# Kernel tuning notes

Measured on AMD Instinct MI355X. Metric: run time of the kernel, lower is better.

Reference implementation:

```python
import jax, jax.numpy as jnp
import numpy as np

# Dims: batch=2, seqlen=L=384, d_inner=d=384, d_state=s=384, dt_rank=r=384, d_conv=4.
# NOTE: the original torch module only runs when L == d_inner == d_state == dt_rank
# (see its broadcasting in SelectiveScan and the Linear layer plumbing); we reproduce
# that exact (quirky) broadcast faithfully.
B_, L_, D_, S_, R_, K_ = 2, 384, 384, 384, 384, 4


def setup_inputs() -> dict:
    key = jax.random.key(0)
    ks = jax.random.split(key, 9)
    f32 = jnp.float32
    return {
        "x": jax.random.normal(ks[0], (B_, L_, D_), f32),
        "A_log": jax.random.normal(ks[1], (D_, S_), f32) * 0.02,
        "D": jax.random.normal(ks[2], (D_,), f32) * 0.02,
        "dt_w": jax.random.normal(ks[3], (D_, R_), f32) * 0.02,
        "dt_b": jax.random.normal(ks[4], (D_,), f32) * 0.02,
        "B_w": jax.random.normal(ks[5], (S_, D_), f32) * (1.0 / np.sqrt(D_)),
        "C_w": jax.random.normal(ks[6], (S_, D_), f32) * (1.0 / np.sqrt(D_)),
        "conv_w": jax.random.normal(ks[7], (D_, 1, K_), f32) * (1.0 / np.sqrt(K_)),
        "conv_b": jnp.zeros((D_,), f32),
    }


def _forward(x, A_log, D, dt_w, dt_b, B_w, C_w, conv_w, conv_b):
    b, L, d = x.shape
    A = -jnp.exp(A_log)                       # (d, s)
    dt = jax.nn.softplus(x @ dt_w.T + dt_b)   # (b, L, d)
    x_dbl = x @ B_w.T                         # (b, L, s)
    Bm = x_dbl @ B_w.T                        # (b, L, s)  (module applies B_proj twice)
    Cm = x_dbl @ C_w.T                        # (b, L, s)
    # causal depthwise conv1d: pad (k-1) on the left == torch pad k-1 then [:, :, :L]
    xc = jax.lax.conv_general_dilated(
        x.transpose(0, 2, 1), conv_w, (1,), [(conv_w.shape[-1] - 1, 0)],
        feature_group_count=d, dimension_numbers=("NCH", "OIH", "NCH"))
    xc = xc + conv_b[None, :, None]
    u = jax.nn.silu(xc.transpose(0, 2, 1))    # (b, L, d)
    # selective scan (faithful to the torch SelectiveScan broadcasting)
    deltaA = jnp.exp(dt[..., None] * A[None, None])          # (b, L, d, s)
    deltaB_u = dt[..., None] * Bm[:, None, :, :] * u[..., None]  # (b, L, d, s), needs L==d

    def step(h, inp):
        dA_i, dBu_i, C_i, u_i = inp
        h = dA_i * h + dBu_i                  # (b, d, s)
        y = jnp.sum(h * C_i[:, None, :], -1) + u_i * D  # (b, d)
        return h, y

    h0 = jnp.zeros((b, d, deltaA.shape[-1]), x.dtype)
    xs = (deltaA.transpose(1, 0, 2, 3), deltaB_u.transpose(1, 0, 2, 3),
          Cm.transpose(1, 0, 2), u.transpose(1, 0, 2))
    _, ys = jax.lax.scan(step, h0, xs)        # ys: (L, b, d)
    return ys.transpose(1, 0, 2)


def reference(x, A_log, D, dt_w, dt_b, B_w, C_w, conv_w, conv_b):
    return _forward(x, A_log, D, dt_w, dt_b, B_w, C_w, conv_w, conv_b)
```

## Files before the change

kernel.cpp:

```cpp
#include <hip/hip_runtime.h>
#include <math.h>

#define B_SZ 2
#define L_SZ 384
#define D_SZ 384
#define S_SZ 384
#define BLK_ELEMS (L_SZ * D_SZ)
#define TOT_ELEMS (B_SZ * L_SZ * D_SZ)
#define LOG2E 1.4426950408889634f

typedef __attribute__((ext_vector_type(8))) short bf16x8;
typedef __attribute__((ext_vector_type(4))) float f32x4;
typedef __attribute__((ext_vector_type(2))) unsigned int u32x2;

__device__ __forceinline__ float fexp2(float x) {
  return __builtin_amdgcn_exp2f(x);
}
__device__ __forceinline__ float softplus_f(float z) {
  return (z > 20.f) ? z : log1pf(__expf(z));
}
__device__ __forceinline__ unsigned short f2bf(float f) {
  unsigned int u = __float_as_uint(f);
  return (unsigned short)((u + 0x7FFFu + ((u >> 16) & 1u)) >> 16);
}
#define PIPELINE_FENCE() asm volatile("" ::: "memory")

__device__ __forceinline__ bf16x8 cvt8(const float* p) {
  const f32x4 v0 = *(const f32x4*)p;
  const f32x4 v1 = *(const f32x4*)(p + 4);
  union { unsigned int u[4]; bf16x8 v; } r;
  asm("v_cvt_pk_bf16_f32 %0, %1, %2" : "=v"(r.u[0]) : "v"(v0[0]), "v"(v0[1]));
  asm("v_cvt_pk_bf16_f32 %0, %1, %2" : "=v"(r.u[1]) : "v"(v0[2]), "v"(v0[3]));
  asm("v_cvt_pk_bf16_f32 %0, %1, %2" : "=v"(r.u[2]) : "v"(v1[0]), "v"(v1[1]));
  asm("v_cvt_pk_bf16_f32 %0, %1, %2" : "=v"(r.u[3]) : "v"(v1[2]), "v"(v1[3]));
  return r.v;
}

template <int CTRL>
__device__ __forceinline__ float dpp_mov(float v) {
  return __int_as_float(
      __builtin_amdgcn_update_dpp(0, __float_as_int(v), CTRL, 0xF, 0xF, true));
}

__device__ __forceinline__ float fold_xor16(float r) {
#if __has_builtin(__builtin_amdgcn_permlane16_swap)
  const unsigned ru = __float_as_uint(r);
  u32x2 p = __builtin_amdgcn_permlane16_swap(ru, ru, false, false);
  return __uint_as_float(p[0]) + __uint_as_float(p[1]);
#else
  return r + __shfl_xor(r, 16, 64);
#endif
}
__device__ __forceinline__ float fold_xor32(float r) {
#if __has_builtin(__builtin_amdgcn_permlane32_swap)
  const unsigned ru = __float_as_uint(r);
  u32x2 p = __builtin_amdgcn_permlane32_swap(ru, ru, false, false);
  return __uint_as_float(p[0]) + __uint_as_float(p[1]);
#else
  return r + __shfl_xor(r, 32, 64);
#endif
}

template <int MODE>
__global__ __launch_bounds__(128, 2) void mfma_dual_gemm(
    const void* __restrict__ Av, const float* __restrict__ W1,
    const float* __restrict__ W2, const float* __restrict__ bias,
    float* __restrict__ O1, unsigned short* __restrict__ O2) {
  __shared__ unsigned short sA[32 * 392];
  __shared__ unsigned short sW1[16 * 392];
  __shared__ unsigned short sW2[16 * 392];

  const int t = threadIdx.x;
  const int wv = t >> 6;
  const int lane = t & 63;
  const int nt = blockIdx.x;
  const int mrow = blockIdx.y;

  const float* W1b = W1 + nt * 16 * 384;
  const float* W2b = W2 + nt * 16 * 384;

  if constexpr (MODE == 1) {
    const float* Ab = (const float*)Av + mrow * 32 * 384;
#pragma unroll
    for (int it = 0; it < 12; ++it) {
      const int id = t + it * 128;
      const int row = id / 48, col = id - row * 48;
      *(bf16x8*)&sA[row * 392 + col * 8] = cvt8(Ab + id * 8);
    }
  } else {
    const unsigned short* Ab = (const unsigned short*)Av + mrow * 32 * 384;
#pragma unroll
    for (int it = 0; it < 12; ++it) {
      const int id = t + it * 128;
      const int row = id / 48, col = id - row * 48;
      *(bf16x8*)&sA[row * 392 + col * 8] = *(const bf16x8*)(Ab + id * 8);
    }
  }
#pragma unroll
  for (int it = 0; it < 6; ++it) {
    const int id = t + it * 128;
    const int row = id / 48, col = id - row * 48;
    *(bf16x8*)&sW1[row * 392 + col * 8] = cvt8(W1b + id * 8);
    *(bf16x8*)&sW2[row * 392 + col * 8] = cvt8(W2b + id * 8);
  }
  __syncthreads();

  const int rc = lane & 15;
  const int quad = lane >> 4;
  bf16x8 af[12], w1f[12], w2f[12];
#pragma unroll
  for (int kt = 0; kt < 12; ++kt) {
    af[kt] = *(const bf16x8*)&sA[(wv * 16 + rc) * 392 + quad * 8 + kt * 32];
    w1f[kt] = *(const bf16x8*)&sW1[rc * 392 + quad * 8 + kt * 32];
    w2f[kt] = *(const bf16x8*)&sW2[rc * 392 + quad * 8 + kt * 32];
  }
  PIPELINE_FENCE();
  f32x4 acc1 = {0.f, 0.f, 0.f, 0.f};
  f32x4 acc2 = {0.f, 0.f, 0.f, 0.f};
#pragma unroll
  for (int kt = 0; kt < 12; ++kt) {
    acc1 = __builtin_amdgcn_mfma_f32_16x16x32_bf16(af[kt], w1f[kt], acc1, 0, 0, 0);
    acc2 = __builtin_amdgcn_mfma_f32_16x16x32_bf16(af[kt], w2f[kt], acc2, 0, 0, 0);
  }
  const int col = nt * 16 + rc;
  const int row0 = mrow * 32 + wv * 16 + quad * 4;
  if constexpr (MODE == 1) {
    const float bb = bias[col];
#pragma unroll
    for (int r = 0; r < 4; ++r) {
      O1[(row0 + r) * 384 + col] = softplus_f(acc1[r] + bb);
      O2[(row0 + r) * 384 + col] = f2bf(acc2[r]);
    }
  } else {
#pragma unroll
    for (int r = 0; r < 4; ++r) {
      O1[(row0 + r) * 384 + col] = acc1[r];
      O2[(row0 + r) * 384 + col] = f2bf(acc2[r]);
    }
  }
}

__global__ __launch_bounds__(256) void conv_tr_kernel(
    const float* __restrict__ x, const float* __restrict__ cw,
    const float* __restrict__ cb, const float* __restrict__ dt,
    float* __restrict__ u, float* __restrict__ dt_t,
    float* __restrict__ dtu_t) {
  __shared__ float Tdt[32][33];
  __shared__ float Tdu[32][33];
  const int tx = threadIdx.x;
  const int ty = threadIdx.y;
  const int b = blockIdx.z;
  const int i0 = blockIdx.y * 32;
  const int l0 = blockIdx.x * 32;
  const int gi = i0 + tx;
  const float cbv = cb[gi];
  const float cw0 = cw[gi * 4 + 0], cw1 = cw[gi * 4 + 1];
  const float cw2 = cw[gi * 4 + 2], cw3 = cw[gi * 4 + 3];
#pragma unroll
  for (int r = 0; r < 4; ++r) {
    const int l = l0 + ty + 8 * r;
    float acc = cbv;
    const float x3 = x[(b * L_SZ + l) * D_SZ + gi];
    const float x2 = (l >= 1) ? x[(b * L_SZ + l - 1) * D_SZ + gi] : 0.f;
    const float x1 = (l >= 2) ? x[(b * L_SZ + l - 2) * D_SZ + gi] : 0.f;
    const float x0 = (l >= 3) ? x[(b * L_SZ + l - 3) * D_SZ + gi] : 0.f;
    acc = fmaf(x0, cw0, acc);
    acc = fmaf(x1, cw1, acc);
    acc = fmaf(x2, cw2, acc);
    acc = fmaf(x3, cw3, acc);
    const float uv = acc / (1.f + __expf(-acc));
    const int off = (b * L_SZ + l) * D_SZ + gi;
    u[off] = uv;
    const float dtv = dt[off];
    Tdt[ty + 8 * r][tx] = dtv;
    Tdu[ty + 8 * r][tx] = dtv * uv;
  }
  __syncthreads();
#pragma unroll
  for (int r = 0; r < 4; ++r) {
    const int il = ty + 8 * r;
    const int off = (b * D_SZ + i0 + il) * L_SZ + l0 + tx;
    dt_t[off] = Tdt[tx][il];
    dtu_t[off] = Tdu[tx][il];
  }
}

struct CChunk {
  unsigned int c[8];
};
struct SChunk {
  f32x4 d0, d1, u0, u1;
};

#define LOAD_CHUNK(K, B0, B1, B2)                                              \
  {                                                                            \
    asm volatile("global_load_ushort %0, %1, off" : "=v"(K.c[0]) : "v"(B0));   \
    asm volatile("global_load_ushort %0, %1, off offset:768"                   \
                 : "=v"(K.c[1]) : "v"(B0));                                    \
    asm volatile("global_load_ushort %0, %1, off offset:1536"                  \
                 : "=v"(K.c[2]) : "v"(B0));                                    \
    asm volatile("global_load_ushort %0, %1, off" : "=v"(K.c[3]) : "v"(B1));   \
    asm volatile("global_load_ushort %0, %1, off offset:768"                   \
                 : "=v"(K.c[4]) : "v"(B1));                                    \
    asm volatile("global_load_ushort %0, %1, off offset:1536"                  \
                 : "=v"(K.c[5]) : "v"(B1));                                    \
    asm volatile("global_load_ushort %0, %1, off" : "=v"(K.c[6]) : "v"(B2));   \
    asm volatile("global_load_ushort %0, %1, off offset:768"                   \
                 : "=v"(K.c[7]) : "v"(B2));                                    \
  }

#define WAIT_CHUNK(K)                                                          \
  asm volatile("s_waitcnt vmcnt(16)"                                           \
               : "+v"(K.c[0]), "+v"(K.c[1]), "+v"(K.c[2]), "+v"(K.c[3]),       \
                 "+v"(K.c[4]), "+v"(K.c[5]), "+v"(K.c[6]), "+v"(K.c[7]))

#define SLOAD_CHUNK(S, SDT, SDU)                                               \
  asm volatile("s_load_dwordx4 %0, %4, 0x0\n\t"                                \
               "s_load_dwordx4 %1, %4, 0x10\n\t"                               \
               "s_load_dwordx4 %2, %5, 0x0\n\t"                                \
               "s_load_dwordx4 %3, %5, 0x10"                                   \
               : "=&s"(S.d0), "=&s"(S.d1), "=&s"(S.u0), "=&s"(S.u1)            \
               : "s"(SDT), "s"(SDU));

#define SWAIT(S)                                                               \
  asm volatile("s_waitcnt lgkmcnt(0)"                                          \
               : "+s"(S.d0), "+s"(S.d1), "+s"(S.u0), "+s"(S.u1))

#define ADV_BASES()                                                            \
  { cb0 += 3072; cb1 += 3072; cb2 += 3072; }
#define SADV()                                                                 \
  { sdt += 8; sdu += 8; }

__global__ __launch_bounds__(64, 4) void scan_kernel(
    const float* __restrict__ A_log, const float* __restrict__ dt_t,
    const float* __restrict__ dtu_t, const float* __restrict__ Bm,
    const unsigned short* __restrict__ Cmbf, float* __restrict__ part) {
  const int bid = blockIdx.x;
  const int xcd = bid & 7;
  const int slot = bid >> 3;
  const int sid = xcd * 96 + slot / 6;
  const int w = slot % 6;
  const int lane = threadIdx.x;
  const int b = sid / D_SZ;
  const int i = sid % D_SZ;
  const int j = w * 64 + lane;

  const float a2 = -__expf(A_log[i * S_SZ + j]) * LOG2E;
  const float bw = Bm[(b * D_SZ + i) * S_SZ + j];
  float h = 0.f;

  const float* sdt = dt_t + (b * D_SZ + i) * L_SZ;
  const float* sdu = dtu_t + (b * D_SZ + i) * L_SZ;
  const unsigned short* cmrow = Cmbf + b * BLK_ELEMS + j;
  const unsigned short* cb0 = cmrow;
  const unsigned short* cb1 = cmrow + 3 * S_SZ;
  const unsigned short* cb2 = cmrow + 6 * S_SZ;

  const int sq = (((lane >> 3) & 1) << 2) | (((lane >> 2) & 1) << 1) | (lane & 1);
  const bool storer = (lane & 0x32) == 0;
  float* pstore = part + ((w * B_SZ + b) * D_SZ + i) * L_SZ + sq;

  asm volatile("" :: "v"(a2), "v"(bw));
  asm volatile("s_waitcnt vmcnt(0)");

  auto compute_chunk = [&](CChunk& K, SChunk& S) {
    float acc[8];
    const float dts[8] = {S.d0[0], S.d0[1], S.d0[2], S.d0[3],
                          S.d1[0], S.d1[1], S.d1[2], S.d1[3]};
    const float dus[8] = {S.u0[0], S.u0[1], S.u0[2], S.u0[3],
                          S.u1[0], S.u1[1], S.u1[2], S.u1[3]};
#pragma unroll
    for (int s = 0; s < 8; ++s) {
      const float e = fexp2(dts[s] * a2);
      h = fmaf(e, h, bw * dus[s]);
      acc[s] = h * __uint_as_float(K.c[s] << 16);
    }
    {
      const bool hi = (lane & 8) != 0;
#pragma unroll
      for (int q = 0; q < 4; ++q) {
        const float keep = hi ? acc[q + 4] : acc[q];
        const float send = hi ? acc[q] : acc[q + 4];
        acc[q] = keep + dpp_mov<0x140>(send);
      }
    }
    {
      const bool hi = (lane & 4) != 0;
#pragma unroll
      for (int q = 0; q < 2; ++q) {
        const float keep = hi ? acc[q + 2] : acc[q];
        const float send = hi ? acc[q] : acc[q + 2];
        acc[q] = keep + dpp_mov<0x141>(send);
      }
    }
    {
      const bool hi = (lane & 1) != 0;
      const float keep = hi ? acc[1] : acc[0];
      const float send = hi ? acc[0] : acc[1];
      acc[0] = keep + dpp_mov<0xB1>(send);
    }
    float r = acc[0];
    r += dpp_mov<0x4E>(r);
    r = fold_xor16(r);
    r = fold_xor32(r);
    if (storer) *pstore = r;
    pstore += 8;
  };

  CChunk K0, K1, K2;
  SChunk S0, S1;
  LOAD_CHUNK(K0, cb0, cb1, cb2);
  ADV_BASES();
  LOAD_CHUNK(K1, cb0, cb1, cb2);
  ADV_BASES();
  SLOAD_CHUNK(S0, sdt, sdu);
  SADV();

#define STEP(KC, SC, SN)                                                       \
  LOAD_CHUNK(KC, cb0, cb1, cb2);                                               \
  ADV_BASES();                                                                 \
  WAIT_CHUNK(KC##_wait);                                                       \
  SWAIT(SC);                                                                   \
  SLOAD_CHUNK(SN, sdt, sdu);                                                   \
  SADV();                                                                      \
  compute_chunk(KC##_wait, SC);

#pragma unroll 1
  for (int it = 0; it < 8; ++it) {
    { CChunk& K2_wait = K0; STEP(K2, S0, S1); }
    { CChunk& K0_wait = K1; STEP(K0, S1, S0); }
    { CChunk& K1_wait = K2; STEP(K1, S0, S1); }
    { CChunk& K2_wait = K0; STEP(K2, S1, S0); }
    { CChunk& K0_wait = K1; STEP(K0, S0, S1); }
    { CChunk& K1_wait = K2; STEP(K1, S1, S0); }
  }
#undef STEP
}

__global__ __launch_bounds__(256) void combine_kernel(
    const float* __restrict__ part, const float* __restrict__ u,
    const float* __restrict__ Dv, float* __restrict__ y) {
  __shared__ float T[32][33];
  const int tx = threadIdx.x;
  const int ty0 = threadIdx.y;
  const int b = blockIdx.z;
  const int i0 = blockIdx.y * 32;
  const int l0 = blockIdx.x * 32;
#pragma unroll
  for (int r = 0; r < 4; ++r) {
    const int il = ty0 + 8 * r;
    float s = 0.f;
#pragma unroll
    for (int w = 0; w < 6; ++w)
      s += part[((w * B_SZ + b) * D_SZ + i0 + il) * L_SZ + l0 + tx];
    T[il][tx] = s;
  }
  __syncthreads();
#pragma unroll
  for (int r = 0; r < 4; ++r) {
    const int ll = ty0 + 8 * r;
    const int gi = i0 + tx;
    const int off = (b * L_SZ + l0 + ll) * D_SZ + gi;
    y[off] = fmaf(u[off], Dv[gi], T[tx][ll]);
  }
}

extern "C" void kernel_launch(void* const* d_in, const int* in_sizes, int n_in,
                              void* d_out, int out_size, void* d_ws,
                              size_t ws_size, hipStream_t stream) {
  const float* x = (const float*)d_in[0];
  const float* A_log = (const float*)d_in[1];
  const float* D = (const float*)d_in[2];
  const float* dt_w = (const float*)d_in[3];
  const float* dt_b = (const float*)d_in[4];
  const float* B_w = (const float*)d_in[5];
  const float* C_w = (const float*)d_in[6];
  const float* conv_w = (const float*)d_in[7];
  const float* conv_b = (const float*)d_in[8];
  float* y = (float*)d_out;

  float* ws = (float*)d_ws;
  float* dt = ws;
  float* u = ws + TOT_ELEMS;
  float* Bm = ws + 2 * TOT_ELEMS;
  float* dt_t = ws + 3 * TOT_ELEMS;
  float* dtu_t = ws + 4 * TOT_ELEMS;
  float* part = ws + 5 * TOT_ELEMS;
  unsigned short* bfarea = (unsigned short*)(ws + 11 * TOT_ELEMS);
  unsigned short* Cmbf = bfarea;
  unsigned short* xdblbf = bfarea + TOT_ELEMS;

  mfma_dual_gemm<1><<<dim3(24, 24), 128, 0, stream>>>(x, dt_w, B_w, dt_b, dt, xdblbf);
  mfma_dual_gemm<2><<<dim3(24, 24), 128, 0, stream>>>(xdblbf, B_w, C_w, nullptr, Bm, Cmbf);
  conv_tr_kernel<<<dim3(L_SZ / 32, D_SZ / 32, B_SZ), dim3(32, 8), 0, stream>>>(
      x, conv_w, conv_b, dt, u, dt_t, dtu_t);
  scan_kernel<<<4608, 64, 0, stream>>>(A_log, dt_t, dtu_t, Bm, Cmbf, part);
  combine_kernel<<<dim3(L_SZ / 32, D_SZ / 32, B_SZ), dim3(32, 8), 0, stream>>>(
      part, u, D, y);
}
```

Before: 131.7 us.

## Pack Cm bf16 into interleaved 4-row quads for vector loads in scan

The second GEMM now writes Cm as packed groups of four consecutive rows per column (8-byte units), so the scan kernel can fetch four timesteps of C with one 64-bit load instead of individual ushort loads. The scan replaces its hand-written inline-asm triple-buffered ushort load pipeline with plain C++ double-buffered u32x2 loads and unpacks bf16 halves via shift/mask. This cuts the number of load instructions in the inner loop, but hands prefetch scheduling to the compiler, which may insert conservative waits and expose load latency.

Result: faster. 128.1 us (-2.7%).

```diff
diff --git a/kernel.cpp b/kernel.cpp
--- a/kernel.cpp
+++ b/kernel.cpp
@@ -65,7 +65,7 @@
 __global__ __launch_bounds__(128, 2) void mfma_dual_gemm(
     const void* __restrict__ Av, const float* __restrict__ W1,
     const float* __restrict__ W2, const float* __restrict__ bias,
-    float* __restrict__ O1, unsigned short* __restrict__ O2) {
+    float* __restrict__ O1, void* __restrict__ O2v) {
   __shared__ unsigned short sA[32 * 392];
   __shared__ unsigned short sW1[16 * 392];
   __shared__ unsigned short sW2[16 * 392];
@@ -125,6 +125,7 @@
   const int col = nt * 16 + rc;
   const int row0 = mrow * 32 + wv * 16 + quad * 4;
   if constexpr (MODE == 1) {
+    unsigned short* O2 = (unsigned short*)O2v;
     const float bb = bias[col];
 #pragma unroll
     for (int r = 0; r < 4; ++r) {
@@ -133,10 +134,14 @@
     }
   } else {
 #pragma unroll
-    for (int r = 0; r < 4; ++r) {
+    for (int r = 0; r < 4; ++r)
       O1[(row0 + r) * 384 + col] = acc1[r];
-      O2[(row0 + r) * 384 + col] = f2bf(acc2[r]);
-    }
+    const unsigned int p01 =
+        (unsigned int)f2bf(acc2[0]) | ((unsigned int)f2bf(acc2[1]) << 16);
+    const unsigned int p23 =
+        (unsigned int)f2bf(acc2[2]) | ((unsigned int)f2bf(acc2[3]) << 16);
+    u32x2 q = {p01, p23};
+    *((u32x2*)O2v + ((row0 >> 2) * 384 + col)) = q;
   }
 }
 
@@ -185,34 +190,9 @@
   }
 }
 
-struct CChunk {
-  unsigned int c[8];
-};
 struct SChunk {
   f32x4 d0, d1, u0, u1;
 };
-
-#define LOAD_CHUNK(K, B0, B1, B2)                                              \
-  {                                                                            \
-    asm volatile("global_load_ushort %0, %1, off" : "=v"(K.c[0]) : "v"(B0));   \
-    asm volatile("global_load_ushort %0, %1, off offset:768"                   \
-                 : "=v"(K.c[1]) : "v"(B0));                                    \
-    asm volatile("global_load_ushort %0, %1, off offset:1536"                  \
-                 : "=v"(K.c[2]) : "v"(B0));                                    \
-    asm volatile("global_load_ushort %0, %1, off" : "=v"(K.c[3]) : "v"(B1));   \
-    asm volatile("global_load_ushort %0, %1, off offset:768"                   \
-                 : "=v"(K.c[4]) : "v"(B1));                                    \
-    asm volatile("global_load_ushort %0, %1, off offset:1536"                  \
-                 : "=v"(K.c[5]) : "v"(B1));                                    \
-    asm volatile("global_load_ushort %0, %1, off" : "=v"(K.c[6]) : "v"(B2));   \
-    asm volatile("global_load_ushort %0, %1, off offset:768"                   \
-                 : "=v"(K.c[7]) : "v"(B2));                                    \
-  }
-
-#define WAIT_CHUNK(K)                                                          \
-  asm volatile("s_waitcnt vmcnt(16)"                                           \
-               : "+v"(K.c[0]), "+v"(K.c[1]), "+v"(K.c[2]), "+v"(K.c[3]),       \
-                 "+v"(K.c[4]), "+v"(K.c[5]), "+v"(K.c[6]), "+v"(K.c[7]))
 
 #define SLOAD_CHUNK(S, SDT, SDU)                                               \
   asm volatile("s_load_dwordx4 %0, %4, 0x0\n\t"                                \
@@ -226,15 +206,13 @@
   asm volatile("s_waitcnt lgkmcnt(0)"                                          \
                : "+s"(S.d0), "+s"(S.d1), "+s"(S.u0), "+s"(S.u1))
 
-#define ADV_BASES()                                                            \
-  { cb0 += 3072; cb1 += 3072; cb2 += 3072; }
 #define SADV()                                                                 \
   { sdt += 8; sdu += 8; }
 
 __global__ __launch_bounds__(64, 4) void scan_kernel(
     const float* __restrict__ A_log, const float* __restrict__ dt_t,
     const float* __restrict__ dtu_t, const float* __restrict__ Bm,
-    const unsigned short* __restrict__ Cmbf, float* __restrict__ part) {
+    const u32x2* __restrict__ Cmq, float* __restrict__ part) {
   const int bid = blockIdx.x;
   const int xcd = bid & 7;
   const int slot = bid >> 3;
@@ -251,29 +229,26 @@
 
   const float* sdt = dt_t + (b * D_SZ + i) * L_SZ;
   const float* sdu = dtu_t + (b * D_SZ + i) * L_SZ;
-  const unsigned short* cmrow = Cmbf + b * BLK_ELEMS + j;
-  const unsigned short* cb0 = cmrow;
-  const unsigned short* cb1 = cmrow + 3 * S_SZ;
-  const unsigned short* cb2 = cmrow + 6 * S_SZ;
+  const u32x2* cq = Cmq + (b * 96) * 384 + j;
 
   const int sq = (((lane >> 3) & 1) << 2) | (((lane >> 2) & 1) << 1) | (lane & 1);
   const bool storer = (lane & 0x32) == 0;
   float* pstore = part + ((w * B_SZ + b) * D_SZ + i) * L_SZ + sq;
 
-  asm volatile("" :: "v"(a2), "v"(bw));
-  asm volatile("s_waitcnt vmcnt(0)");
-
-  auto compute_chunk = [&](CChunk& K, SChunk& S) {
+  auto compute_chunk = [&](u32x2 qa_c, u32x2 qb_c, SChunk& S) {
     float acc[8];
     const float dts[8] = {S.d0[0], S.d0[1], S.d0[2], S.d0[3],
                           S.d1[0], S.d1[1], S.d1[2], S.d1[3]};
     const float dus[8] = {S.u0[0], S.u0[1], S.u0[2], S.u0[3],
                           S.u1[0], S.u1[1], S.u1[2], S.u1[3]};
+    const unsigned int qs[4] = {qa_c[0], qa_c[1], qb_c[0], qb_c[1]};
 #pragma unroll
     for (int s = 0; s < 8; ++s) {
       const float e = fexp2(dts[s] * a2);
       h = fmaf(e, h, bw * dus[s]);
-      acc[s] = h * __uint_as_float(K.c[s] << 16);
+      const unsigned int cw32 =
+          (s & 1) ? (qs[s >> 1] & 0xFFFF0000u) : (qs[s >> 1] << 16);
+      acc[s] = h * __uint_as_float(cw32);
     }
     {
       const bool hi = (lane & 8) != 0;
@@ -307,32 +282,32 @@
     pstore += 8;
   };
 
-  CChunk K0, K1, K2;
   SChunk S0, S1;
-  LOAD_CHUNK(K0, cb0, cb1, cb2);
-  ADV_BASES();
-  LOAD_CHUNK(K1, cb0, cb1, cb2);
-  ADV_BASES();
-  SLOAD_CHUNK(S0, sdt, sdu);
-  SADV();
-
-#define STEP(KC, SC, SN)                                                       \
-  LOAD_CHUNK(KC, cb0, cb1, cb2);                                               \
-  ADV_BASES();                                                                 \
-  WAIT_CHUNK(KC##_wait);                                                       \
-  SWAIT(SC);                                                                   \
-  SLOAD_CHUNK(SN, sdt, sdu);                                                   \
-  SADV();                                                                      \
-  compute_chunk(KC##_wait, SC);
+  u32x2 qa = cq[0], qb = cq[384];
+  cq += 768;
+  SLOAD_CHUNK(S0, sdt, sdu); SADV();
+
+#define STEP(SC, SN)                                                           \
+  {                                                                            \
+    const u32x2 qa_n = cq[0];                                                  \
+    const u32x2 qb_n = cq[384];                                                \
+    cq += 768;                                                                 \
+    SWAIT(SC);                                                                 \
+    SLOAD_CHUNK(SN, sdt, sdu);                                                 \
+    SADV();                                                                    \
+    compute_chunk(qa, qb, SC);                                                 \
+    qa = qa_n;                                                                 \
+    qb = qb_n;                                                                 \
+  }
 
 #pragma unroll 1
   for (int it = 0; it < 8; ++it) {
-    { CChunk& K2_wait = K0; STEP(K2, S0, S1); }
-    { CChunk& K0_wait = K1; STEP(K0, S1, S0); }
-    { CChunk& K1_wait = K2; STEP(K1, S0, S1); }
-    { CChunk& K2_wait = K0; STEP(K2, S1, S0); }
-    { CChunk& K0_wait = K1; STEP(K0, S0, S1); }
-    { CChunk& K1_wait = K2; STEP(K1, S1, S0); }
+    STEP(S0, S1);
+    STEP(S1, S0);
+    STEP(S0, S1);
+    STEP(S1, S0);
+    STEP(S0, S1);
+    STEP(S1, S0);
   }
 #undef STEP
 }
@@ -387,14 +362,14 @@
   float* dtu_t = ws + 4 * TOT_ELEMS;
   float* part = ws + 5 * TOT_ELEMS;
   unsigned short* bfarea = (unsigned short*)(ws + 11 * TOT_ELEMS);
-  unsigned short* Cmbf = bfarea;
+  u32x2* Cmq = (u32x2*)bfarea;
   unsigned short* xdblbf = bfarea + TOT_ELEMS;
 
   mfma_dual_gemm<1><<<dim3(24, 24), 128, 0, stream>>>(x, dt_w, B_w, dt_b, dt, xdblbf);
-  mfma_dual_gemm<2><<<dim3(24, 24), 128, 0, stream>>>(xdblbf, B_w, C_w, nullptr, Bm, Cmbf);
+  mfma_dual_gemm<2><<<dim3(24, 24), 128, 0, stream>>>(xdblbf, B_w, C_w, nullptr, Bm, Cmq);
   conv_tr_kernel<<<dim3(L_SZ / 32, D_SZ / 32, B_SZ), dim3(32, 8), 0, stream>>>(
       x, conv_w, conv_b, dt, u, dt_t, dtu_t);
-  scan_kernel<<<4608, 64, 0, stream>>>(A_log, dt_t, dtu_t, Bm, Cmbf, part);
+  scan_kernel<<<4608, 64, 0, stream>>>(A_log, dt_t, dtu_t, Bm, Cmq, part);
   combine_kernel<<<dim3(L_SZ / 32, D_SZ / 32, B_SZ), dim3(32, 8), 0, stream>>>(
       part, u, D, y);
 }
```
